# Optimization experiments

Hardware: AMD Instinct MI355X
Metric: run time of the kernel (lower is better)

## Reference

```python
import jax, jax.numpy as jnp
import numpy as np

L, H, N = 8192, 1024, 1024
MAX_PHASE = 6.283


def setup_inputs() -> dict:
    key = jax.random.key(0)
    ks = jax.random.split(key, 9)
    input_real = jax.random.uniform(ks[0], (L, H), dtype=jnp.float32)
    input_imag = jax.random.uniform(ks[1], (L, H), dtype=jnp.float32)
    # LRU parameter init (r_min=0, r_max=1, max_phase=6.283)
    u1 = jax.random.uniform(ks[2], (N,), dtype=jnp.float32)
    u2 = jax.random.uniform(ks[3], (N,), dtype=jnp.float32)
    nu_log = jnp.log(-0.5 * jnp.log(u1))
    theta_log = jnp.log(u2 * MAX_PHASE)
    B_real = jax.random.normal(ks[4], (N, H), dtype=jnp.float32) / np.float32(np.sqrt(2 * H))
    B_imag = jax.random.normal(ks[5], (N, H), dtype=jnp.float32) / np.float32(np.sqrt(2 * H))
    C_real = jax.random.normal(ks[6], (H, N), dtype=jnp.float32) / np.float32(np.sqrt(N))
    C_imag = jax.random.normal(ks[7], (H, N), dtype=jnp.float32) / np.float32(np.sqrt(N))
    D = jax.random.normal(ks[8], (H,), dtype=jnp.float32)
    diag_lambda = jnp.exp(jax.lax.complex(-jnp.exp(nu_log), jnp.exp(theta_log)))
    gamma_log = jnp.log(jnp.sqrt(1.0 - jnp.abs(diag_lambda) ** 2))
    return dict(input_real=input_real, input_imag=input_imag,
                nu_log=nu_log, theta_log=theta_log,
                B_real=B_real, B_imag=B_imag,
                C_real=C_real, C_imag=C_imag,
                D=D, gamma_log=gamma_log)


def _binop(e_i, e_j):
    a_i, bu_i = e_i
    a_j, bu_j = e_j
    return a_j * a_i, a_j * bu_i + bu_j


def _lru_forward(input_real, input_imag, nu_log, theta_log,
                 B_real, B_imag, C_real, C_imag, D, gamma_log):
    u = jax.lax.complex(input_real, input_imag)                      # (L, H) complex
    Lambda = jnp.exp(jax.lax.complex(-jnp.exp(nu_log), jnp.exp(theta_log)))  # (N,)
    # Faithful to source: exp(i * gamma_log), NOT exp(gamma_log)
    exp_gamma = jnp.exp(jax.lax.complex(jnp.zeros_like(gamma_log), gamma_log))  # (N,)
    B_norm = jax.lax.complex(B_real, B_imag) * exp_gamma[:, None]    # (N, H)
    Bu = jnp.einsum('lh,nh->ln', u, B_norm)                          # (L, N)
    Lambda_el = jnp.broadcast_to(Lambda[None, :], Bu.shape)          # (L, N)
    _, x = jax.lax.associative_scan(_binop, (Lambda_el, Bu))         # (L, N) states
    C = jax.lax.complex(C_real, C_imag)                              # (H, N)
    Dc = D.astype(C.dtype)                                           # (H,) complex
    y = jnp.real(jnp.einsum('ln,hn->lh', x, C)) + jnp.real(Dc[None, :] * u)
    return y                                                         # (L, H) float32


def reference(input_real, input_imag, nu_log, theta_log,
              B_real, B_imag, C_real, C_imag, D, gamma_log):
    return _lru_forward(input_real, input_imag, nu_log, theta_log,
                        B_real, B_imag, C_real, C_imag, D, gamma_log)
```

## Files before the change

kernel.cpp:

```cpp
#include <hip/hip_runtime.h>
#include <math.h>

#define L_SEQ 8192
#define H_DIM 1024
#define N_DIM 1024
#define K2    2048
#define NCHUNK 256
#define CHUNK 32

typedef unsigned short u16;
typedef __attribute__((ext_vector_type(8))) __bf16 bf16x8;
typedef __attribute__((ext_vector_type(4))) float  f32x4;

__device__ __forceinline__ u16 f2bf(float x) {
    unsigned int u = __float_as_uint(x);
    u = (u + 0x7fffu + ((u >> 16) & 1u)) >> 16;
    return (u16)u;
}
__device__ __forceinline__ float bf2f(u16 h) {
    return __uint_as_float(((unsigned int)h) << 16);
}

__device__ __forceinline__ void gload_lds16(const void* g, void* s) {
    __builtin_amdgcn_global_load_lds(
        (const __attribute__((address_space(1))) unsigned int*)g,
        (__attribute__((address_space(3))) unsigned int*)s, 16, 0, 0);
}

__global__ void pack_u(const float* __restrict__ R, const float* __restrict__ I,
                       u16* __restrict__ A) {
    size_t t = (size_t)blockIdx.x * 256 + threadIdx.x;
    size_t base = t * 4;
    int lrow = (int)(base >> 10);
    int h    = (int)(base & 1023);
    float4 r  = *reinterpret_cast<const float4*>(R + base);
    float4 im = *reinterpret_cast<const float4*>(I + base);
    u16* p0 = A + ((size_t)lrow << 11) + h;
    *reinterpret_cast<ushort4*>(p0) =
        make_ushort4(f2bf(r.x), f2bf(r.y), f2bf(r.z), f2bf(r.w));
    *reinterpret_cast<ushort4*>(p0 + 1024) =
        make_ushort4(f2bf(im.x), f2bf(im.y), f2bf(im.z), f2bf(im.w));
}

__global__ void bnorm_pack(const float* __restrict__ Br, const float* __restrict__ Bi,
                           const float* __restrict__ G, u16* __restrict__ Bp) {
    size_t t = (size_t)blockIdx.x * 256 + threadIdx.x;
    size_t base = t * 4;
    int n = (int)(base >> 10);
    int h = (int)(base & 1023);
    float g = G[n];
    float sg, cg;
    sincosf(g, &sg, &cg);
    float4 br = *reinterpret_cast<const float4*>(Br + base);
    float4 bi = *reinterpret_cast<const float4*>(Bi + base);
    float nr0 = br.x * cg - bi.x * sg, ni0 = br.x * sg + bi.x * cg;
    float nr1 = br.y * cg - bi.y * sg, ni1 = br.y * sg + bi.y * cg;
    float nr2 = br.z * cg - bi.z * sg, ni2 = br.z * sg + bi.z * cg;
    float nr3 = br.w * cg - bi.w * sg, ni3 = br.w * sg + bi.w * cg;
    u16* row0 = Bp + (size_t)n * K2;
    u16* row1 = Bp + (size_t)(N_DIM + n) * K2;
    *reinterpret_cast<ushort4*>(row0 + h) =
        make_ushort4(f2bf(nr0), f2bf(nr1), f2bf(nr2), f2bf(nr3));
    *reinterpret_cast<ushort4*>(row0 + 1024 + h) =
        make_ushort4(f2bf(-ni0), f2bf(-ni1), f2bf(-ni2), f2bf(-ni3));
    *reinterpret_cast<ushort4*>(row1 + h) =
        make_ushort4(f2bf(ni0), f2bf(ni1), f2bf(ni2), f2bf(ni3));
    *reinterpret_cast<ushort4*>(row1 + 1024 + h) =
        make_ushort4(f2bf(nr0), f2bf(nr1), f2bf(nr2), f2bf(nr3));
}

__global__ void pack_C(const float* __restrict__ Cr, const float* __restrict__ Ci,
                       u16* __restrict__ Cp) {
    size_t t = (size_t)blockIdx.x * 256 + threadIdx.x;
    size_t base = t * 4;
    int h = (int)(base >> 10);
    int n = (int)(base & 1023);
    float4 cr = *reinterpret_cast<const float4*>(Cr + base);
    float4 ci = *reinterpret_cast<const float4*>(Ci + base);
    u16* row = Cp + (size_t)h * K2;
    *reinterpret_cast<ushort4*>(row + n) =
        make_ushort4(f2bf(cr.x), f2bf(cr.y), f2bf(cr.z), f2bf(cr.w));
    *reinterpret_cast<ushort4*>(row + 1024 + n) =
        make_ushort4(f2bf(-ci.x), f2bf(-ci.y), f2bf(-ci.z), f2bf(-ci.w));
}

__global__ __launch_bounds__(512, 2) void gemm_pipe(
    const u16* __restrict__ A, const u16* __restrict__ B, int Klen, int lda,
    u16* __restrict__ OutB, int ldo) {
    constexpr int ABYTES = 256 * 128;
    constexpr int SLOT   = 2 * ABYTES;
    __shared__ __attribute__((aligned(128))) char lds[2 * SLOT];
    const int tid = threadIdx.x;
    const int l   = tid & 63;
    const int w   = tid >> 6;
    const int wm  = w >> 2;
    const int wn  = w & 3;
    const long bm = (long)blockIdx.x * 256;
    const long bn = (long)blockIdx.y * 256;

    f32x4 acc[8][4];
#pragma unroll
    for (int i = 0; i < 8; ++i)
#pragma unroll
        for (int j = 0; j < 4; ++j) acc[i][j] = (f32x4){0.f, 0.f, 0.f, 0.f};

    const int    lr        = tid >> 3;
    const int    swzcol    = (((tid & 7) ^ (lr & 7)) << 4);
    const size_t rowstride = (size_t)lda * 2;
    const size_t a_src0    = (size_t)(bm + lr) * rowstride + swzcol;
    const size_t b_src0    = (size_t)(bn + lr) * rowstride + swzcol;
    const char*  Agb       = (const char*)A;
    const char*  Bgb       = (const char*)B;
    const int nt = Klen / 64;

    auto STAGE_A = [&](int kt, int h) {
        if (kt >= nt) return;
        const size_t kofs = (size_t)kt * 128;
        char* d = lds + (kt & 1) * SLOT + h * 16384 + tid * 16;
#pragma unroll
        for (int j = 0; j < 2; ++j)
            gload_lds16(Agb + a_src0 + (size_t)(h * 128 + j * 64) * rowstride + kofs,
                        d + j * 8192);
    };
    auto STAGE_B = [&](int kt, int h) {
        if (kt >= nt) return;
        const size_t kofs = (size_t)kt * 128;
        char* d = lds + (kt & 1) * SLOT + ABYTES + h * 16384 + tid * 16;
#pragma unroll
        for (int j = 0; j < 2; ++j)
            gload_lds16(Bgb + b_src0 + (size_t)(h * 128 + j * 64) * rowstride + kofs,
                        d + j * 8192);
    };

    const int l15   = l & 15;
    const int lslot = l >> 4;

    auto READ_A = [&](bf16x8 (&af)[8], const char* lA, int kk) {
#pragma unroll
        for (int mi = 0; mi < 8; ++mi) {
            int r   = wm * 128 + mi * 16 + l15;
            int sl3 = ((kk << 2) | lslot) ^ (r & 7);
            af[mi]  = *reinterpret_cast<const bf16x8*>(lA + r * 128 + sl3 * 16);
        }
    };
    auto READ_B = [&](bf16x8 (&bg)[4], const char* lB, int kk) {
#pragma unroll
        for (int ni = 0; ni < 4; ++ni) {
            int r   = wn * 64 + ni * 16 + l15;
            int sl3 = ((kk << 2) | lslot) ^ (r & 7);
            bg[ni]  = *reinterpret_cast<const bf16x8*>(lB + r * 128 + sl3 * 16);
        }
    };
    auto MFMA_Q = [&](bf16x8 (&af)[8], bf16x8 (&bg)[4], int qn) {
        __builtin_amdgcn_s_setprio(1);
#pragma unroll
        for (int mi = 0; mi < 8; ++mi)
#pragma unroll
            for (int nj = 0; nj < 2; ++nj)
                acc[mi][qn * 2 + nj] = __builtin_amdgcn_mfma_f32_16x16x32_bf16(
                    af[mi], bg[qn * 2 + nj], acc[mi][qn * 2 + nj], 0, 0, 0);
        __builtin_amdgcn_s_setprio(0);
    };

#define SBAR  do { __builtin_amdgcn_sched_barrier(0);                        \
    __builtin_amdgcn_s_barrier();                                            \
    __builtin_amdgcn_sched_barrier(0); } while (0)
#define LGKM0 do { asm volatile("s_waitcnt lgkmcnt(0)" ::: "memory");        \
    __builtin_amdgcn_sched_barrier(0); } while (0)

    STAGE_A(0, 0); STAGE_B(0, 0); STAGE_A(0, 1); STAGE_B(0, 1);
    STAGE_A(1, 0); STAGE_B(1, 0);
    asm volatile("s_waitcnt vmcnt(4)" ::: "memory");
    SBAR;

    bf16x8 af0[8], af1[8], bg0[4], bg1[4];

    for (int t = 0; t < nt; ++t) {
        const char* lA = lds + (t & 1) * SLOT;
        const char* lB = lA + ABYTES;
        READ_A(af0, lA, 0);
        READ_B(bg0, lB, 0);
        STAGE_A(t + 1, 1);
        LGKM0;
        MFMA_Q(af0, bg0, 0);
        READ_A(af1, lA, 1);
        READ_B(bg1, lB, 1);
        STAGE_B(t + 1, 1);
        MFMA_Q(af0, bg0, 1);
        LGKM0;
        SBAR;
        STAGE_A(t + 2, 0);
        MFMA_Q(af1, bg1, 0);
        STAGE_B(t + 2, 0);
        MFMA_Q(af1, bg1, 1);
        if (t < nt - 2) asm volatile("s_waitcnt vmcnt(4)" ::: "memory");
        else            asm volatile("s_waitcnt vmcnt(0)" ::: "memory");
        SBAR;
    }
#undef SBAR
#undef LGKM0

#pragma unroll
    for (int mi = 0; mi < 8; ++mi) {
        const long row0 = bm + wm * 128 + mi * 16 + ((l >> 4) << 2);
#pragma unroll
        for (int ni = 0; ni < 4; ++ni) {
            const long col = bn + wn * 64 + ni * 16 + l15;
#pragma unroll
            for (int r = 0; r < 4; ++r)
                OutB[(size_t)(row0 + r) * ldo + col] = f2bf(acc[mi][ni][r]);
        }
    }
}

__global__ __launch_bounds__(256, 2) void gemm_small(
    const u16* __restrict__ A, const u16* __restrict__ B, int Klen, int lda,
    float* __restrict__ OutF, int ldo,
    const float* __restrict__ Dv, const float* __restrict__ Ur) {
    constexpr int ABYTES = 128 * 128;
    constexpr int SLOT   = 2 * ABYTES;
    __shared__ __attribute__((aligned(128))) char lds[2 * SLOT];
    const int tid = threadIdx.x;
    const int l   = tid & 63;
    const int w   = tid >> 6;
    const int wm  = w >> 1;
    const int wn  = w & 1;
    const long bm = (long)blockIdx.x * 128;
    const long bn = (long)blockIdx.y * 128;

    f32x4 acc[4][4];
#pragma unroll
    for (int i = 0; i < 4; ++i)
#pragma unroll
        for (int j = 0; j < 4; ++j) acc[i][j] = (f32x4){0.f, 0.f, 0.f, 0.f};

    const int    lr        = tid >> 3;
    const int    swzcol    = (((tid & 7) ^ (lr & 7)) << 4);
    const size_t rowstride = (size_t)lda * 2;
    const size_t a_src0    = (size_t)(bm + lr) * rowstride + swzcol;
    const size_t b_src0    = (size_t)(bn + lr) * rowstride + swzcol;
    const char*  Agb       = (const char*)A;
    const char*  Bgb       = (const char*)B;

    auto STAGE = [&](int kt, int sl) {
        const size_t kofs = (size_t)kt * 128;
        char* la = lds + sl * SLOT + tid * 16;
        char* lb = lds + sl * SLOT + ABYTES + tid * 16;
#pragma unroll
        for (int j = 0; j < 4; ++j)
            gload_lds16(Agb + a_src0 + (size_t)j * 32 * rowstride + kofs,
                        la + j * 4096);
#pragma unroll
        for (int j = 0; j < 4; ++j)
            gload_lds16(Bgb + b_src0 + (size_t)j * 32 * rowstride + kofs,
                        lb + j * 4096);
    };

    const int l15   = l & 15;
    const int lslot = l >> 4;

    const int nt = Klen / 64;
    STAGE(0, 0);
    STAGE(1, 1);

    for (int t = 0; t < nt; ++t) {
        const int s = t & 1;
        if (t < nt - 1) asm volatile("s_waitcnt vmcnt(8)" ::: "memory");
        else            asm volatile("s_waitcnt vmcnt(0)" ::: "memory");
        __builtin_amdgcn_sched_barrier(0);
        __builtin_amdgcn_s_barrier();
        __builtin_amdgcn_sched_barrier(0);

        const char* lA = lds + s * SLOT;
        const char* lB = lA + ABYTES;
#pragma unroll
        for (int kk = 0; kk < 2; ++kk) {
            bf16x8 af[4], bg[4];
#pragma unroll
            for (int mi = 0; mi < 4; ++mi) {
                int r   = wm * 64 + mi * 16 + l15;
                int sl3 = ((kk << 2) | lslot) ^ (r & 7);
                af[mi]  = *reinterpret_cast<const bf16x8*>(lA + r * 128 + sl3 * 16);
            }
#pragma unroll
            for (int ni = 0; ni < 4; ++ni) {
                int r   = wn * 64 + ni * 16 + l15;
                int sl3 = ((kk << 2) | lslot) ^ (r & 7);
                bg[ni]  = *reinterpret_cast<const bf16x8*>(lB + r * 128 + sl3 * 16);
            }
            __builtin_amdgcn_s_setprio(1);
#pragma unroll
            for (int mi = 0; mi < 4; ++mi)
#pragma unroll
                for (int ni = 0; ni < 4; ++ni)
                    acc[mi][ni] = __builtin_amdgcn_mfma_f32_16x16x32_bf16(
                        af[mi], bg[ni], acc[mi][ni], 0, 0, 0);
            __builtin_amdgcn_s_setprio(0);
        }
        __builtin_amdgcn_sched_barrier(0);
        __builtin_amdgcn_s_barrier();
        __builtin_amdgcn_sched_barrier(0);
        if (t + 2 < nt) STAGE(t + 2, s);
    }

#pragma unroll
    for (int mi = 0; mi < 4; ++mi) {
        const long row0 = bm + wm * 64 + mi * 16 + ((l >> 4) << 2);
#pragma unroll
        for (int ni = 0; ni < 4; ++ni) {
            const long col = bn + wn * 64 + ni * 16 + l15;
            const float d = Dv[col];
#pragma unroll
            for (int r = 0; r < 4; ++r) {
                size_t o = (size_t)(row0 + r) * ldo + col;
                OutF[o] = acc[mi][ni][r] + d * Ur[o];
            }
        }
    }
}

__global__ void scan_sum(const u16* __restrict__ X,
                         const float* __restrict__ nu_log,
                         const float* __restrict__ theta_log,
                         float* __restrict__ Acr, float* __restrict__ Aci,
                         float* __restrict__ bcr, float* __restrict__ bci) {
    int n0 = (blockIdx.y * 256 + threadIdx.x) * 2;
    int c  = blockIdx.x;
    float lr0, li0, lr1, li1;
    {
        float m0 = expf(-expf(nu_log[n0]));
        float t0 = expf(theta_log[n0]);
        float s0, c0; sincosf(t0, &s0, &c0);
        lr0 = m0 * c0; li0 = m0 * s0;
        float m1 = expf(-expf(nu_log[n0 + 1]));
        float t1 = expf(theta_log[n0 + 1]);
        float s1, c1; sincosf(t1, &s1, &c1);
        lr1 = m1 * c1; li1 = m1 * s1;
    }
    float sr0 = 0.f, si0 = 0.f, pr0 = 1.f, pi0 = 0.f;
    float sr1 = 0.f, si1 = 0.f, pr1 = 1.f, pi1 = 0.f;
    size_t base = (size_t)c * CHUNK * K2 + n0;
    for (int j = 0; j < CHUNK; ++j) {
        size_t idx = base + (size_t)j * K2;
        unsigned int ru = *reinterpret_cast<const unsigned int*>(X + idx);
        unsigned int iu = *reinterpret_cast<const unsigned int*>(X + idx + 1024);
        float br0 = bf2f((u16)ru), br1 = bf2f((u16)(ru >> 16));
        float bi0 = bf2f((u16)iu), bi1 = bf2f((u16)(iu >> 16));
        float nr0 = lr0 * sr0 - li0 * si0 + br0;
        float ni0 = lr0 * si0 + li0 * sr0 + bi0;
        sr0 = nr0; si0 = ni0;
        float nr1 = lr1 * sr1 - li1 * si1 + br1;
        float ni1 = lr1 * si1 + li1 * sr1 + bi1;
        sr1 = nr1; si1 = ni1;
        float q0 = lr0 * pr0 - li0 * pi0, q1 = lr0 * pi0 + li0 * pr0;
        pr0 = q0; pi0 = q1;
        float q2 = lr1 * pr1 - li1 * pi1, q3 = lr1 * pi1 + li1 * pr1;
        pr1 = q2; pi1 = q3;
    }
    Acr[c * N_DIM + n0] = pr0; Aci[c * N_DIM + n0] = pi0;
    bcr[c * N_DIM + n0] = sr0; bci[c * N_DIM + n0] = si0;
    Acr[c * N_DIM + n0 + 1] = pr1; Aci[c * N_DIM + n0 + 1] = pi1;
    bcr[c * N_DIM + n0 + 1] = sr1; bci[c * N_DIM + n0 + 1] = si1;
}

__global__ void scan_carry(const float* __restrict__ Acr, const float* __restrict__ Aci,
                           const float* __restrict__ bcr, const float* __restrict__ bci,
                           float* __restrict__ car, float* __restrict__ cai) {
    int n = blockIdx.x * 256 + threadIdx.x;
    float sr = 0.f, si = 0.f;
    for (int c = 0; c < NCHUNK; ++c) {
        car[c * N_DIM + n] = sr; cai[c * N_DIM + n] = si;
        float ar = Acr[c * N_DIM + n], ai = Aci[c * N_DIM + n];
        float nr = ar * sr - ai * si + bcr[c * N_DIM + n];
        float ni = ar * si + ai * sr + bci[c * N_DIM + n];
        sr = nr; si = ni;
    }
}

__global__ void scan_apply(u16* __restrict__ X,
                           const float* __restrict__ nu_log,
                           const float* __restrict__ theta_log,
                           const float* __restrict__ car, const float* __restrict__ cai) {
    int n0 = (blockIdx.y * 256 + threadIdx.x) * 2;
    int c  = blockIdx.x;
    float lr0, li0, lr1, li1;
    {
        float m0 = expf(-expf(nu_log[n0]));
        float t0 = expf(theta_log[n0]);
        float s0, c0; sincosf(t0, &s0, &c0);
        lr0 = m0 * c0; li0 = m0 * s0;
        float m1 = expf(-expf(nu_log[n0 + 1]));
        float t1 = expf(theta_log[n0 + 1]);
        float s1, c1; sincosf(t1, &s1, &c1);
        lr1 = m1 * c1; li1 = m1 * s1;
    }
    float sr0 = car[c * N_DIM + n0],     si0 = cai[c * N_DIM + n0];
    float sr1 = car[c * N_DIM + n0 + 1], si1 = cai[c * N_DIM + n0 + 1];
    size_t base = (size_t)c * CHUNK * K2 + n0;
    for (int j = 0; j < CHUNK; ++j) {
        size_t idx = base + (size_t)j * K2;
        unsigned int ru = *reinterpret_cast<const unsigned int*>(X + idx);
        unsigned int iu = *reinterpret_cast<const unsigned int*>(X + idx + 1024);
        float br0 = bf2f((u16)ru), br1 = bf2f((u16)(ru >> 16));
        float bi0 = bf2f((u16)iu), bi1 = bf2f((u16)(iu >> 16));
        float nr0 = lr0 * sr0 - li0 * si0 + br0;
        float ni0 = lr0 * si0 + li0 * sr0 + bi0;
        sr0 = nr0; si0 = ni0;
        float nr1 = lr1 * sr1 - li1 * si1 + br1;
        float ni1 = lr1 * si1 + li1 * sr1 + bi1;
        sr1 = nr1; si1 = ni1;
        *reinterpret_cast<unsigned int*>(X + idx) =
            (unsigned int)f2bf(sr0) | ((unsigned int)f2bf(sr1) << 16);
        *reinterpret_cast<unsigned int*>(X + idx + 1024) =
            (unsigned int)f2bf(si0) | ((unsigned int)f2bf(si1) << 16);
    }
}

extern "C" void kernel_launch(void* const* d_in, const int* in_sizes, int n_in,
                              void* d_out, int out_size, void* d_ws, size_t ws_size,
                              hipStream_t stream) {
    (void)in_sizes; (void)n_in; (void)out_size; (void)ws_size;
    const float* input_real = (const float*)d_in[0];
    const float* input_imag = (const float*)d_in[1];
    const float* nu_log     = (const float*)d_in[2];
    const float* theta_log  = (const float*)d_in[3];
    const float* B_real     = (const float*)d_in[4];
    const float* B_imag     = (const float*)d_in[5];
    const float* C_real     = (const float*)d_in[6];
    const float* C_imag     = (const float*)d_in[7];
    const float* D          = (const float*)d_in[8];
    const float* gamma_log  = (const float*)d_in[9];
    float* y = (float*)d_out;

    char* ws = (char*)d_ws;
    u16* Ap   = (u16*)(ws + ((size_t)2 << 20));
    u16* Cp   = Ap;
    u16* Bp   = (u16*)(ws + ((size_t)34 << 20));
    float* Acr = (float*)(ws + ((size_t)34 << 20));
    float* Aci = Acr + NCHUNK * N_DIM;
    float* bcr = Aci + NCHUNK * N_DIM;
    float* bci = bcr + NCHUNK * N_DIM;
    float* car = bci + NCHUNK * N_DIM;
    float* cai = car + NCHUNK * N_DIM;
    u16* X    = (u16*)(ws + ((size_t)42 << 20));

    pack_u<<<(L_SEQ * H_DIM / 4) / 256, 256, 0, stream>>>(input_real, input_imag, Ap);
    bnorm_pack<<<(N_DIM * H_DIM / 4) / 256, 256, 0, stream>>>(B_real, B_imag, gamma_log, Bp);
    gemm_pipe<<<dim3(L_SEQ / 256, K2 / 256), 512, 0, stream>>>(
        Ap, Bp, K2, K2, X, K2);
    scan_sum<<<dim3(NCHUNK, N_DIM / 512), 256, 0, stream>>>(
        X, nu_log, theta_log, Acr, Aci, bcr, bci);
    scan_carry<<<N_DIM / 256, 256, 0, stream>>>(Acr, Aci, bcr, bci, car, cai);
    scan_apply<<<dim3(NCHUNK, N_DIM / 512), 256, 0, stream>>>(
        X, nu_log, theta_log, car, cai);
    pack_C<<<(H_DIM * N_DIM / 4) / 256, 256, 0, stream>>>(C_real, C_imag, Cp);
    gemm_small<<<dim3(L_SEQ / 128, H_DIM / 128), 256, 0, stream>>>(
        X, Cp, K2, K2, y, H_DIM, D, input_real);
}
```

Measured before the change: 170.7 us.

## Interleave half-tile loads with MFMA in gemm_small and parallelize carry scan

The small GEMM's main loop now issues half-tile global-to-LDS loads interleaved with LDS reads and quarter MFMA groups, so memory traffic overlaps compute instead of being separated by two barriers per k-step. Separately, the chunk carry scan, previously a serial 256-step loop per state, becomes a wave-level parallel prefix scan using shuffles. It computes Lambda^CHUNK analytically instead of storing per-chunk decay products, which drops those arrays. Chunk sums and carries are stored transposed (state-major) so each wave reads them contiguously, while scan_sum and scan_apply now make strided single-float accesses. The closed-form Lambda power and the extra shuffle work may change numerics slightly.

```diff
diff --git a/kernel.cpp b/kernel.cpp
--- a/kernel.cpp
+++ b/kernel.cpp
@@ -241,67 +241,94 @@
     const size_t b_src0    = (size_t)(bn + lr) * rowstride + swzcol;
     const char*  Agb       = (const char*)A;
     const char*  Bgb       = (const char*)B;
-
-    auto STAGE = [&](int kt, int sl) {
+    const int nt = Klen / 64;
+
+    auto STAGE_A = [&](int kt, int h) {
+        if (kt >= nt) return;
         const size_t kofs = (size_t)kt * 128;
-        char* la = lds + sl * SLOT + tid * 16;
-        char* lb = lds + sl * SLOT + ABYTES + tid * 16;
-#pragma unroll
-        for (int j = 0; j < 4; ++j)
-            gload_lds16(Agb + a_src0 + (size_t)j * 32 * rowstride + kofs,
-                        la + j * 4096);
-#pragma unroll
-        for (int j = 0; j < 4; ++j)
-            gload_lds16(Bgb + b_src0 + (size_t)j * 32 * rowstride + kofs,
-                        lb + j * 4096);
+        char* d = lds + (kt & 1) * SLOT + h * 8192 + tid * 16;
+#pragma unroll
+        for (int j = 0; j < 2; ++j)
+            gload_lds16(Agb + a_src0 + (size_t)(h * 64 + j * 32) * rowstride + kofs,
+                        d + j * 4096);
+    };
+    auto STAGE_B = [&](int kt, int h) {
+        if (kt >= nt) return;
+        const size_t kofs = (size_t)kt * 128;
+        char* d = lds + (kt & 1) * SLOT + ABYTES + h * 8192 + tid * 16;
+#pragma unroll
+        for (int j = 0; j < 2; ++j)
+            gload_lds16(Bgb + b_src0 + (size_t)(h * 64 + j * 32) * rowstride + kofs,
+                        d + j * 4096);
     };
 
     const int l15   = l & 15;
     const int lslot = l >> 4;
 
-    const int nt = Klen / 64;
-    STAGE(0, 0);
-    STAGE(1, 1);
+    auto READ_A = [&](bf16x8 (&af)[4], const char* lA, int kk) {
+#pragma unroll
+        for (int mi = 0; mi < 4; ++mi) {
+            int r   = wm * 64 + mi * 16 + l15;
+            int sl3 = ((kk << 2) | lslot) ^ (r & 7);
+            af[mi]  = *reinterpret_cast<const bf16x8*>(lA + r * 128 + sl3 * 16);
+        }
+    };
+    auto READ_B = [&](bf16x8 (&bg)[4], const char* lB, int kk) {
+#pragma unroll
+        for (int ni = 0; ni < 4; ++ni) {
+            int r   = wn * 64 + ni * 16 + l15;
+            int sl3 = ((kk << 2) | lslot) ^ (r & 7);
+            bg[ni]  = *reinterpret_cast<const bf16x8*>(lB + r * 128 + sl3 * 16);
+        }
+    };
+    auto MFMA_Q = [&](bf16x8 (&af)[4], bf16x8 (&bg)[4], int qn) {
+        __builtin_amdgcn_s_setprio(1);
+#pragma unroll
+        for (int mi = 0; mi < 4; ++mi)
+#pragma unroll
+            for (int nj = 0; nj < 2; ++nj)
+                acc[mi][qn * 2 + nj] = __builtin_amdgcn_mfma_f32_16x16x32_bf16(
+                    af[mi], bg[qn * 2 + nj], acc[mi][qn * 2 + nj], 0, 0, 0);
+        __builtin_amdgcn_s_setprio(0);
+    };
+
+#define SBAR  do { __builtin_amdgcn_sched_barrier(0);                        \
+    __builtin_amdgcn_s_barrier();                                            \
+    __builtin_amdgcn_sched_barrier(0); } while (0)
+#define LGKM0 do { asm volatile("s_waitcnt lgkmcnt(0)" ::: "memory");        \
+    __builtin_amdgcn_sched_barrier(0); } while (0)
+
+    STAGE_A(0, 0); STAGE_B(0, 0); STAGE_A(0, 1); STAGE_B(0, 1);
+    STAGE_A(1, 0); STAGE_B(1, 0);
+    asm volatile("s_waitcnt vmcnt(4)" ::: "memory");
+    SBAR;
+
+    bf16x8 af0[4], af1[4], bg0[4], bg1[4];
 
     for (int t = 0; t < nt; ++t) {
-        const int s = t & 1;
-        if (t < nt - 1) asm volatile("s_waitcnt vmcnt(8)" ::: "memory");
+        const char* lA = lds + (t & 1) * SLOT;
+        const char* lB = lA + ABYTES;
+        READ_A(af0, lA, 0);
+        READ_B(bg0, lB, 0);
+        STAGE_A(t + 1, 1);
+        LGKM0;
+        MFMA_Q(af0, bg0, 0);
+        READ_A(af1, lA, 1);
+        READ_B(bg1, lB, 1);
+        STAGE_B(t + 1, 1);
+        MFMA_Q(af0, bg0, 1);
+        LGKM0;
+        SBAR;
+        STAGE_A(t + 2, 0);
+        MFMA_Q(af1, bg1, 0);
+        STAGE_B(t + 2, 0);
+        MFMA_Q(af1, bg1, 1);
+        if (t < nt - 2) asm volatile("s_waitcnt vmcnt(4)" ::: "memory");
         else            asm volatile("s_waitcnt vmcnt(0)" ::: "memory");
-        __builtin_amdgcn_sched_barrier(0);
-        __builtin_amdgcn_s_barrier();
-        __builtin_amdgcn_sched_barrier(0);
-
-        const char* lA = lds + s * SLOT;
-        const char* lB = lA + ABYTES;
-#pragma unroll
-        for (int kk = 0; kk < 2; ++kk) {
-            bf16x8 af[4], bg[4];
-#pragma unroll
-            for (int mi = 0; mi < 4; ++mi) {
-                int r   = wm * 64 + mi * 16 + l15;
-                int sl3 = ((kk << 2) | lslot) ^ (r & 7);
-                af[mi]  = *reinterpret_cast<const bf16x8*>(lA + r * 128 + sl3 * 16);
-            }
-#pragma unroll
-            for (int ni = 0; ni < 4; ++ni) {
-                int r   = wn * 64 + ni * 16 + l15;
-                int sl3 = ((kk << 2) | lslot) ^ (r & 7);
-                bg[ni]  = *reinterpret_cast<const bf16x8*>(lB + r * 128 + sl3 * 16);
-            }
-            __builtin_amdgcn_s_setprio(1);
-#pragma unroll
-            for (int mi = 0; mi < 4; ++mi)
-#pragma unroll
-                for (int ni = 0; ni < 4; ++ni)
-                    acc[mi][ni] = __builtin_amdgcn_mfma_f32_16x16x32_bf16(
-                        af[mi], bg[ni], acc[mi][ni], 0, 0, 0);
-            __builtin_amdgcn_s_setprio(0);
-        }
-        __builtin_amdgcn_sched_barrier(0);
-        __builtin_amdgcn_s_barrier();
-        __builtin_amdgcn_sched_barrier(0);
-        if (t + 2 < nt) STAGE(t + 2, s);
-    }
+        SBAR;
+    }
+#undef SBAR
+#undef LGKM0
 
 #pragma unroll
     for (int mi = 0; mi < 4; ++mi) {
@@ -322,7 +349,6 @@
 __global__ void scan_sum(const u16* __restrict__ X,
                          const float* __restrict__ nu_log,
                          const float* __restrict__ theta_log,
-                         float* __restrict__ Acr, float* __restrict__ Aci,
                          float* __restrict__ bcr, float* __restrict__ bci) {
     int n0 = (blockIdx.y * 256 + threadIdx.x) * 2;
     int c  = blockIdx.x;
@@ -337,8 +363,7 @@
         float s1, c1; sincosf(t1, &s1, &c1);
         lr1 = m1 * c1; li1 = m1 * s1;
     }
-    float sr0 = 0.f, si0 = 0.f, pr0 = 1.f, pi0 = 0.f;
-    float sr1 = 0.f, si1 = 0.f, pr1 = 1.f, pi1 = 0.f;
+    float sr0 = 0.f, si0 = 0.f, sr1 = 0.f, si1 = 0.f;
     size_t base = (size_t)c * CHUNK * K2 + n0;
     for (int j = 0; j < CHUNK; ++j) {
         size_t idx = base + (size_t)j * K2;
@@ -352,29 +377,57 @@
         float nr1 = lr1 * sr1 - li1 * si1 + br1;
         float ni1 = lr1 * si1 + li1 * sr1 + bi1;
         sr1 = nr1; si1 = ni1;
-        float q0 = lr0 * pr0 - li0 * pi0, q1 = lr0 * pi0 + li0 * pr0;
-        pr0 = q0; pi0 = q1;
-        float q2 = lr1 * pr1 - li1 * pi1, q3 = lr1 * pi1 + li1 * pr1;
-        pr1 = q2; pi1 = q3;
-    }
-    Acr[c * N_DIM + n0] = pr0; Aci[c * N_DIM + n0] = pi0;
-    bcr[c * N_DIM + n0] = sr0; bci[c * N_DIM + n0] = si0;
-    Acr[c * N_DIM + n0 + 1] = pr1; Aci[c * N_DIM + n0 + 1] = pi1;
-    bcr[c * N_DIM + n0 + 1] = sr1; bci[c * N_DIM + n0 + 1] = si1;
-}
-
-__global__ void scan_carry(const float* __restrict__ Acr, const float* __restrict__ Aci,
-                           const float* __restrict__ bcr, const float* __restrict__ bci,
+    }
+    bcr[(size_t)n0 * NCHUNK + c] = sr0; bci[(size_t)n0 * NCHUNK + c] = si0;
+    bcr[(size_t)(n0 + 1) * NCHUNK + c] = sr1; bci[(size_t)(n0 + 1) * NCHUNK + c] = si1;
+}
+
+__global__ void scan_carry(const float* __restrict__ bcr, const float* __restrict__ bci,
+                           const float* __restrict__ nu_log,
+                           const float* __restrict__ theta_log,
                            float* __restrict__ car, float* __restrict__ cai) {
-    int n = blockIdx.x * 256 + threadIdx.x;
-    float sr = 0.f, si = 0.f;
-    for (int c = 0; c < NCHUNK; ++c) {
-        car[c * N_DIM + n] = sr; cai[c * N_DIM + n] = si;
-        float ar = Acr[c * N_DIM + n], ai = Aci[c * N_DIM + n];
-        float nr = ar * sr - ai * si + bcr[c * N_DIM + n];
-        float ni = ar * si + ai * sr + bci[c * N_DIM + n];
-        sr = nr; si = ni;
-    }
+    const int lane = threadIdx.x & 63;
+    const int n    = blockIdx.x * 4 + (threadIdx.x >> 6);
+    float mag = expf(-(float)CHUNK * expf(nu_log[n]));
+    float ang = (float)CHUNK * expf(theta_log[n]);
+    float sL, cL; sincosf(ang, &sL, &cL);
+    const float Lr = mag * cL, Li = mag * sL;
+    const size_t base = (size_t)n * NCHUNK + lane * 4;
+    float4 br4 = *reinterpret_cast<const float4*>(bcr + base);
+    float4 bi4 = *reinterpret_cast<const float4*>(bci + base);
+    float br = br4.x, bi = bi4.x;
+    { float tr = Lr * br - Li * bi + br4.y, ti = Lr * bi + Li * br + bi4.y; br = tr; bi = ti; }
+    { float tr = Lr * br - Li * bi + br4.z, ti = Lr * bi + Li * br + bi4.z; br = tr; bi = ti; }
+    { float tr = Lr * br - Li * bi + br4.w, ti = Lr * bi + Li * br + bi4.w; br = tr; bi = ti; }
+    float L2r = Lr * Lr - Li * Li, L2i = 2.f * Lr * Li;
+    float Ar = L2r * L2r - L2i * L2i, Ai = 2.f * L2r * L2i;
+#pragma unroll
+    for (int d = 1; d < 64; d <<= 1) {
+        float pAr = __shfl_up(Ar, d);
+        float pAi = __shfl_up(Ai, d);
+        float pbr = __shfl_up(br, d);
+        float pbi = __shfl_up(bi, d);
+        if (lane >= d) {
+            float nbr = Ar * pbr - Ai * pbi + br;
+            float nbi = Ar * pbi + Ai * pbr + bi;
+            float nAr = Ar * pAr - Ai * pAi;
+            float nAi = Ar * pAi + Ai * pAr;
+            br = nbr; bi = nbi; Ar = nAr; Ai = nAi;
+        }
+    }
+    float sr = __shfl_up(br, 1);
+    float si = __shfl_up(bi, 1);
+    if (lane == 0) { sr = 0.f; si = 0.f; }
+    float4 or4, oi4;
+    or4.x = sr; oi4.x = si;
+    { float tr = Lr * sr - Li * si + br4.x, ti = Lr * si + Li * sr + bi4.x; sr = tr; si = ti; }
+    or4.y = sr; oi4.y = si;
+    { float tr = Lr * sr - Li * si + br4.y, ti = Lr * si + Li * sr + bi4.y; sr = tr; si = ti; }
+    or4.z = sr; oi4.z = si;
+    { float tr = Lr * sr - Li * si + br4.z, ti = Lr * si + Li * sr + bi4.z; sr = tr; si = ti; }
+    or4.w = sr; oi4.w = si;
+    *reinterpret_cast<float4*>(car + base) = or4;
+    *reinterpret_cast<float4*>(cai + base) = oi4;
 }
 
 __global__ void scan_apply(u16* __restrict__ X,
@@ -394,8 +447,8 @@
         float s1, c1; sincosf(t1, &s1, &c1);
         lr1 = m1 * c1; li1 = m1 * s1;
     }
-    float sr0 = car[c * N_DIM + n0],     si0 = cai[c * N_DIM + n0];
-    float sr1 = car[c * N_DIM + n0 + 1], si1 = cai[c * N_DIM + n0 + 1];
+    float sr0 = car[(size_t)n0 * NCHUNK + c],       si0 = cai[(size_t)n0 * NCHUNK + c];
+    float sr1 = car[(size_t)(n0 + 1) * NCHUNK + c], si1 = cai[(size_t)(n0 + 1) * NCHUNK + c];
     size_t base = (size_t)c * CHUNK * K2 + n0;
     for (int j = 0; j < CHUNK; ++j) {
         size_t idx = base + (size_t)j * K2;
@@ -436,9 +489,7 @@
     u16* Ap   = (u16*)(ws + ((size_t)2 << 20));
     u16* Cp   = Ap;
     u16* Bp   = (u16*)(ws + ((size_t)34 << 20));
-    float* Acr = (float*)(ws + ((size_t)34 << 20));
-    float* Aci = Acr + NCHUNK * N_DIM;
-    float* bcr = Aci + NCHUNK * N_DIM;
+    float* bcr = (float*)(ws + ((size_t)34 << 20));
     float* bci = bcr + NCHUNK * N_DIM;
     float* car = bci + NCHUNK * N_DIM;
     float* cai = car + NCHUNK * N_DIM;
@@ -449,8 +500,8 @@
     gemm_pipe<<<dim3(L_SEQ / 256, K2 / 256), 512, 0, stream>>>(
         Ap, Bp, K2, K2, X, K2);
     scan_sum<<<dim3(NCHUNK, N_DIM / 512), 256, 0, stream>>>(
-        X, nu_log, theta_log, Acr, Aci, bcr, bci);
-    scan_carry<<<N_DIM / 256, 256, 0, stream>>>(Acr, Aci, bcr, bci, car, cai);
+        X, nu_log, theta_log, bcr, bci);
+    scan_carry<<<N_DIM / 4, 256, 0, stream>>>(bcr, bci, nu_log, theta_log, car, cai);
     scan_apply<<<dim3(NCHUNK, N_DIM / 512), 256, 0, stream>>>(
         X, nu_log, theta_log, car, cai);
     pack_C<<<(H_DIM * N_DIM / 4) / 256, 256, 0, stream>>>(C_real, C_imag, Cp);
```

New measurement: 153.7 us. -10.0%, faster.
